# Performance work log

Hardware: AMD Instinct MI355X
Metric: run time of the kernel (lower is better)

Reference implementation:

```python
import jax, jax.numpy as jnp
import numpy as np

N = 50000      # nodes
E = 800000     # edges (before self-loops)
DIN = 64
DH = 64
DOUT = 64
G = 500        # graphs in batch
EPS = 1e-5     # BatchNorm eps


def setup_inputs() -> dict:
    key = jax.random.key(0)
    ks = jax.random.split(key, 8)
    x = jax.random.normal(ks[0], (N, DIN), dtype=jnp.float32)
    edge_index = jax.random.randint(ks[1], (2, E), 0, N, dtype=jnp.int32)
    batch = jnp.sort(jax.random.randint(ks[2], (N,), 0, G, dtype=jnp.int32))

    def lin(k, di, do):
        return (jax.random.normal(k, (di, do), dtype=jnp.float32) / np.float32(np.sqrt(di)))

    inp = dict(x=x, edge_index=edge_index, batch=batch)
    dims = [(DIN, DH), (DH, DH), (DH, DOUT)]
    for i, (di, do) in enumerate(dims, start=1):
        inp[f"W{i}"] = lin(ks[2 + i], di, do)
        inp[f"b{i}"] = jnp.zeros((do,), jnp.float32)
        inp[f"gamma{i}"] = jnp.ones((do,), jnp.float32)
        inp[f"beta{i}"] = jnp.zeros((do,), jnp.float32)
    return inp


def _gcn_norm(edge_index, n_nodes):
    # add self loops, compute symmetric normalization deg^-1/2 * deg^-1/2
    loop = jnp.arange(n_nodes, dtype=edge_index.dtype)
    src = jnp.concatenate([edge_index[0], loop])
    dst = jnp.concatenate([edge_index[1], loop])
    deg = jax.ops.segment_sum(jnp.ones_like(dst, dtype=jnp.float32), dst,
                              num_segments=n_nodes)
    dinv = jax.lax.rsqrt(deg)  # deg >= 1 thanks to self-loops
    norm = dinv[src] * dinv[dst]  # [E + N]
    return src, dst, norm


def _gcn_conv(x, src, dst, norm, W, b, n_nodes):
    h = x @ W                               # [N, dout]
    msg = h[src] * norm[:, None]            # gather + scale  [E+N, dout]
    out = jax.ops.segment_sum(msg, dst, num_segments=n_nodes)  # scatter-add
    return out + b


def _batchnorm(x, gamma, beta):
    mean = jnp.mean(x, axis=0)
    var = jnp.mean(jnp.square(x - mean), axis=0)  # biased, as in torch training BN
    return gamma * (x - mean) * jax.lax.rsqrt(var + EPS) + beta


def reference(x, edge_index, batch, W1, b1, gamma1, beta1,
              W2, b2, gamma2, beta2, W3, b3, gamma3, beta3):
    src, dst, norm = _gcn_norm(edge_index, N)
    layers = [(W1, b1, gamma1, beta1), (W2, b2, gamma2, beta2),
              (W3, b3, gamma3, beta3)]
    h = x
    for i, (W, b, g, be) in enumerate(layers):
        h = _gcn_conv(h, src, dst, norm, W, b, N)
        h = _batchnorm(h, g, be)
        if i < len(layers) - 1:
            h = jax.nn.relu(h)  # dropout is identity in eval / reference
    # global mean pool over graphs
    sums = jax.ops.segment_sum(h, batch, num_segments=G)          # [G, DOUT]
    cnts = jax.ops.segment_sum(jnp.ones((N,), jnp.float32), batch,
                               num_segments=G)
    return sums / jnp.maximum(cnts, 1.0)[:, None]
```

## Files before the change

kernel.cpp:

```cpp
#include <hip/hip_runtime.h>
#include <hip/hip_fp16.h>

#define BN_EPS 1e-5f
#define CCH 4096
#define NSLICE 32
#define OUT_CAP 8192
#define CAP 8192
#define SXS 68


__device__ inline __half2 u2h(unsigned u) {
    union { unsigned u; __half2 h; } x; x.u = u; return x.h;
}
__device__ inline unsigned h2u(__half2 h) {
    union { unsigned u; __half2 h; } x; x.h = h; return x.u;
}
__device__ inline unsigned pack_f16x2(float a, float b) {
    return h2u(__floats2half2_rn(a, b));
}


__global__ __launch_bounds__(256) void scatter_direct(const int* __restrict__ src,
                                                      const int* __restrict__ dst,
                                                      int* __restrict__ ccnt,
                                                      unsigned* __restrict__ tmp,
                                                      float* __restrict__ cnt_g,
                                                      float* __restrict__ out,
                                                      int E, int G) {
    __shared__ int lcnt[256];
    int t = threadIdx.x;
    int tid = blockIdx.x * 256 + t;
    int stride = gridDim.x * 256;
    for (int i = tid; i < G * 64; i += stride) out[i] = 0.f;
    for (int i = tid; i < G; i += stride) cnt_g[i] = 0.f;

    int e0 = blockIdx.x * CCH;
    lcnt[t] = 0;
    __syncthreads();
#pragma unroll
    for (int k = 0; k < CCH / 256; ++k) {
        int e = e0 + k * 256 + t;
        if (e < E) atomicAdd(&lcnt[dst[e] >> 8], 1);
    }
    __syncthreads();
    int c = lcnt[t];
    __syncthreads();
    if (c > 0) lcnt[t] = t * CAP + atomicAdd(&ccnt[t], c);
    __syncthreads();
#pragma unroll
    for (int k = 0; k < CCH / 256; ++k) {
        int e = e0 + k * 256 + t;
        if (e < E) {
            int d = dst[e];
            int pos = atomicAdd(&lcnt[d >> 8], 1);
            tmp[pos] = ((unsigned)src[e] << 8) | (unsigned)(d & 255);
        }
    }
}


__global__ __launch_bounds__(256) void build_csr(const unsigned* __restrict__ tmp,
                                                 const int* __restrict__ ccnt,
                                                 int* __restrict__ rp,
                                                 unsigned short* __restrict__ deg,
                                                 unsigned short* __restrict__ col,
                                                 float* __restrict__ dinv,
                                                 const int* __restrict__ batch,
                                                 float* __restrict__ cnt_g,
                                                 int n, int G) {
    __shared__ int hist[256];
    __shared__ int sc[256];
    __shared__ unsigned short outw[OUT_CAP];
    __shared__ int h[512];
    int b = blockIdx.x;
    int t = threadIdx.x;
    int beg = b * CAP;
    int m = ccnt[b];
    int end = beg + m;
    hist[t] = 0;
    __syncthreads();
    for (int e = beg + t; e < end; e += 256) atomicAdd(&hist[tmp[e] & 255u], 1);
    __syncthreads();
    int v = hist[t];
    sc[t] = v;
    __syncthreads();
    for (int off = 1; off < 256; off <<= 1) {
        int u = (t >= off) ? sc[t - off] : 0;
        __syncthreads();
        sc[t] += u;
        __syncthreads();
    }
    int excl = sc[t] - v;
    int node = b * 256 + t;
    if (node < n) {
        dinv[node] = rsqrtf(1.0f + (float)v);
        rp[node] = beg + excl;
        deg[node] = (unsigned short)v;
    }
    hist[t] = excl;
    __syncthreads();
    if (m <= OUT_CAP) {
        for (int e = beg + t; e < end; e += 256) {
            unsigned p = tmp[e];
            int pos = atomicAdd(&hist[p & 255u], 1);
            outw[pos] = (unsigned short)(p >> 8);
        }
        __syncthreads();
        for (int i = t; i < m; i += 256) col[beg + i] = outw[i];
    } else {
        for (int e = beg + t; e < end; e += 256) {
            unsigned p = tmp[e];
            int pos = atomicAdd(&hist[p & 255u], 1);
            col[beg + pos] = (unsigned short)(p >> 8);
        }
    }
    if (G <= 512) {
        __syncthreads();
        for (int i = t; i < 512; i += 256) h[i] = 0;
        __syncthreads();
        for (int i = b * 256 + t; i < n; i += gridDim.x * 256)
            atomicAdd(&h[batch[i]], 1);
        __syncthreads();
        for (int i = t; i < G; i += 256)
            if (h[i]) atomicAdd(&cnt_g[i], (float)h[i]);
    } else {
        for (int i = b * 256 + t; i < n; i += gridDim.x * 256)
            atomicAdd(&cnt_g[batch[i]], 1.0f);
    }
}


__global__ __launch_bounds__(256) void gemm64_v2(const float* __restrict__ X,
                                                 const float* __restrict__ W,
                                                 const float* __restrict__ dinv,
                                                 const float* __restrict__ part,
                                                 const float* __restrict__ gamma,
                                                 const float* __restrict__ beta,
                                                 int has_bn, float inv_n,
                                                 unsigned* __restrict__ Hs, int n) {
    __shared__ float sX[64 * SXS];
    __shared__ float sW[64 * SXS];
    __shared__ float s_scsh[128];
    int t = threadIdx.x;
    int c4 = t & 15;
    int base = blockIdx.x * 64;

    if (has_bn) {
        if (t < 128) {
            float s = 0.f;
#pragma unroll
            for (int k = 0; k < NSLICE; ++k) s += part[k * 128 + t];
            s_scsh[t] = s;
        }
        __syncthreads();
        if (t < 64) {
            float mean = s_scsh[t] * inv_n;
            float var = s_scsh[64 + t] * inv_n - mean * mean;
            float sc = gamma[t] * rsqrtf(var + BN_EPS);
            s_scsh[t] = sc;
            s_scsh[64 + t] = beta[t] - mean * sc;
        }
        __syncthreads();
    }

    {
        const float4* W4 = (const float4*)W;
#pragma unroll
        for (int it = 0; it < 4; ++it) {
            int idx = it * 256 + t;
            int r = idx >> 4;
            float4 v = W4[r * 16 + c4];
            *(float4*)&sW[r * SXS + c4 * 4] = v;
        }
    }
    {
        const float4* X4 = (const float4*)X;
        float4 sc4, sh4;
        if (has_bn) {
            sc4 = *(const float4*)&s_scsh[c4 * 4];
            sh4 = *(const float4*)&s_scsh[64 + c4 * 4];
        }
#pragma unroll
        for (int it = 0; it < 4; ++it) {
            int idx = it * 256 + t;
            int r = idx >> 4;
            int grow = base + r;
            float4 v = make_float4(0.f, 0.f, 0.f, 0.f);
            if (grow < n) v = X4[(size_t)grow * 16 + c4];
            if (has_bn) {
                v.x = fmaxf(fmaf(v.x, sc4.x, sh4.x), 0.f);
                v.y = fmaxf(fmaf(v.y, sc4.y, sh4.y), 0.f);
                v.z = fmaxf(fmaf(v.z, sc4.z, sh4.z), 0.f);
                v.w = fmaxf(fmaf(v.w, sc4.w, sh4.w), 0.f);
            }
            *(float4*)&sX[r * SXS + c4 * 4] = v;
        }
    }
    __syncthreads();

    int rgrp = t >> 4;
    float4 acc[4];
#pragma unroll
    for (int ri = 0; ri < 4; ++ri) acc[ri] = make_float4(0.f, 0.f, 0.f, 0.f);

#pragma unroll 4
    for (int k4 = 0; k4 < 16; ++k4) {
        float4 xv[4], wv[4];
#pragma unroll
        for (int ri = 0; ri < 4; ++ri)
            xv[ri] = *(const float4*)&sX[(rgrp + 16 * ri) * SXS + k4 * 4];
#pragma unroll
        for (int kk = 0; kk < 4; ++kk)
            wv[kk] = *(const float4*)&sW[(k4 * 4 + kk) * SXS + c4 * 4];
#pragma unroll
        for (int ri = 0; ri < 4; ++ri) {
            acc[ri].x = fmaf(xv[ri].x, wv[0].x, acc[ri].x);
            acc[ri].y = fmaf(xv[ri].x, wv[0].y, acc[ri].y);
            acc[ri].z = fmaf(xv[ri].x, wv[0].z, acc[ri].z);
            acc[ri].w = fmaf(xv[ri].x, wv[0].w, acc[ri].w);
            acc[ri].x = fmaf(xv[ri].y, wv[1].x, acc[ri].x);
            acc[ri].y = fmaf(xv[ri].y, wv[1].y, acc[ri].y);
            acc[ri].z = fmaf(xv[ri].y, wv[1].z, acc[ri].z);
            acc[ri].w = fmaf(xv[ri].y, wv[1].w, acc[ri].w);
            acc[ri].x = fmaf(xv[ri].z, wv[2].x, acc[ri].x);
            acc[ri].y = fmaf(xv[ri].z, wv[2].y, acc[ri].y);
            acc[ri].z = fmaf(xv[ri].z, wv[2].z, acc[ri].z);
            acc[ri].w = fmaf(xv[ri].z, wv[2].w, acc[ri].w);
            acc[ri].x = fmaf(xv[ri].w, wv[3].x, acc[ri].x);
            acc[ri].y = fmaf(xv[ri].w, wv[3].y, acc[ri].y);
            acc[ri].z = fmaf(xv[ri].w, wv[3].z, acc[ri].z);
            acc[ri].w = fmaf(xv[ri].w, wv[3].w, acc[ri].w);
        }
    }

#pragma unroll
    for (int ri = 0; ri < 4; ++ri) {
        int row = base + rgrp + 16 * ri;
        if (row < n) {
            float dv = dinv[row];
            uint2 o2;
            o2.x = pack_f16x2(acc[ri].x * dv, acc[ri].y * dv);
            o2.y = pack_f16x2(acc[ri].z * dv, acc[ri].w * dv);
            ((uint2*)Hs)[(size_t)row * 16 + c4] = o2;
        }
    }
}


__global__ __launch_bounds__(256) void agg(const uint4* __restrict__ Hs4,
                                           const int* __restrict__ rp,
                                           const unsigned short* __restrict__ deg,
                                           const unsigned short* __restrict__ col,
                                           const float* __restrict__ dinv,
                                           float* __restrict__ Y,
                                           float* __restrict__ part, int n) {
    __shared__ float sS[4][64];
    __shared__ float sQ[4][64];
    int t = threadIdx.x;
    int w = t >> 6;
    int lane = t & 63;
    int g = lane >> 3;
    int c = lane & 7;
    int d = blockIdx.x * 4 + w;
    bool valid = d < n;
    int dc = valid ? d : 0;
    __half2 a0 = u2h(0u), a1 = u2h(0u), a2 = u2h(0u), a3 = u2h(0u);
    int beg = 0, end = 0;
    if (valid) { beg = rp[dc]; end = beg + (int)deg[dc]; }
    for (int b = beg; b < end; b += 64) {
        int m = min(64, end - b);
        int myidx = (lane < m) ? (int)col[b + lane] : 0;
        int jj = 0;
        for (; jj + 15 < m; jj += 16) {
            int s0 = __shfl(myidx, jj + g, 64);
            int s1 = __shfl(myidx, jj + 8 + g, 64);
            uint4 v0 = Hs4[(size_t)s0 * 8 + c];
            uint4 v1 = Hs4[(size_t)s1 * 8 + c];
            a0 = __hadd2(a0, u2h(v0.x)); a1 = __hadd2(a1, u2h(v0.y));
            a2 = __hadd2(a2, u2h(v0.z)); a3 = __hadd2(a3, u2h(v0.w));
            a0 = __hadd2(a0, u2h(v1.x)); a1 = __hadd2(a1, u2h(v1.y));
            a2 = __hadd2(a2, u2h(v1.z)); a3 = __hadd2(a3, u2h(v1.w));
        }
        for (; jj < m; jj += 8) {
            int e = jj + g;
            int s0 = __shfl(myidx, e, 64);
            if (e < m) {
                uint4 v = Hs4[(size_t)s0 * 8 + c];
                a0 = __hadd2(a0, u2h(v.x)); a1 = __hadd2(a1, u2h(v.y));
                a2 = __hadd2(a2, u2h(v.z)); a3 = __hadd2(a3, u2h(v.w));
            }
        }
    }
#pragma unroll
    for (int mask = 8; mask <= 32; mask <<= 1) {
        a0 = __hadd2(a0, u2h((unsigned)__shfl_xor((int)h2u(a0), mask, 64)));
        a1 = __hadd2(a1, u2h((unsigned)__shfl_xor((int)h2u(a1), mask, 64)));
        a2 = __hadd2(a2, u2h((unsigned)__shfl_xor((int)h2u(a2), mask, 64)));
        a3 = __hadd2(a3, u2h((unsigned)__shfl_xor((int)h2u(a3), mask, 64)));
    }
    if (g == 0) {
        float2 f0 = __half22float2(a0), f1 = __half22float2(a1);
        float2 f2 = __half22float2(a2), f3 = __half22float2(a3);
        float y0 = f0.x, y1 = f0.y, y2 = f1.x, y3 = f1.y;
        float y4 = f2.x, y5 = f2.y, y6 = f3.x, y7 = f3.y;
        if (valid) {
            uint4 hv = Hs4[(size_t)dc * 8 + c];
            float2 h0 = __half22float2(u2h(hv.x)), h1 = __half22float2(u2h(hv.y));
            float2 h2v = __half22float2(u2h(hv.z)), h3 = __half22float2(u2h(hv.w));
            float dv = dinv[dc];
            y0 = (y0 + h0.x) * dv; y1 = (y1 + h0.y) * dv;
            y2 = (y2 + h1.x) * dv; y3 = (y3 + h1.y) * dv;
            y4 = (y4 + h2v.x) * dv; y5 = (y5 + h2v.y) * dv;
            y6 = (y6 + h3.x) * dv; y7 = (y7 + h3.y) * dv;
            *(float4*)&Y[(size_t)dc * 64 + c * 8]     = make_float4(y0, y1, y2, y3);
            *(float4*)&Y[(size_t)dc * 64 + c * 8 + 4] = make_float4(y4, y5, y6, y7);
        } else {
            y0 = y1 = y2 = y3 = y4 = y5 = y6 = y7 = 0.f;
        }
        *(float4*)&sS[w][c * 8]     = make_float4(y0, y1, y2, y3);
        *(float4*)&sS[w][c * 8 + 4] = make_float4(y4, y5, y6, y7);
        *(float4*)&sQ[w][c * 8]     = make_float4(y0 * y0, y1 * y1, y2 * y2, y3 * y3);
        *(float4*)&sQ[w][c * 8 + 4] = make_float4(y4 * y4, y5 * y5, y6 * y6, y7 * y7);
    }
    __syncthreads();
    if (t < 64) {
        float s = sS[0][t] + sS[1][t] + sS[2][t] + sS[3][t];
        float qq = sQ[0][t] + sQ[1][t] + sQ[2][t] + sQ[3][t];
        float* dst = part + (size_t)(blockIdx.x & (NSLICE - 1)) * 128;
        atomicAdd(&dst[t], s);
        atomicAdd(&dst[64 + t], qq);
    }
}

__global__ __launch_bounds__(256) void agg_pool(const uint4* __restrict__ Hs4,
                                                const int* __restrict__ rp,
                                                const unsigned short* __restrict__ deg,
                                                const unsigned short* __restrict__ col,
                                                const float* __restrict__ dinv,
                                                const int* __restrict__ batch,
                                                float* __restrict__ out,
                                                float* __restrict__ part, int n) {
    __shared__ float sS[4][64];
    __shared__ float sQ[4][64];
    __shared__ int sG[4];
    int t = threadIdx.x;
    int w = t >> 6;
    int lane = t & 63;
    int g = lane >> 3;
    int c = lane & 7;
    int d = blockIdx.x * 4 + w;
    bool valid = d < n;
    int dc = valid ? d : 0;
    __half2 a0 = u2h(0u), a1 = u2h(0u), a2 = u2h(0u), a3 = u2h(0u);
    int beg = 0, end = 0;
    if (valid) { beg = rp[dc]; end = beg + (int)deg[dc]; }
    for (int b = beg; b < end; b += 64) {
        int m = min(64, end - b);
        int myidx = (lane < m) ? (int)col[b + lane] : 0;
        int jj = 0;
        for (; jj + 15 < m; jj += 16) {
            int s0 = __shfl(myidx, jj + g, 64);
            int s1 = __shfl(myidx, jj + 8 + g, 64);
            uint4 v0 = Hs4[(size_t)s0 * 8 + c];
            uint4 v1 = Hs4[(size_t)s1 * 8 + c];
            a0 = __hadd2(a0, u2h(v0.x)); a1 = __hadd2(a1, u2h(v0.y));
            a2 = __hadd2(a2, u2h(v0.z)); a3 = __hadd2(a3, u2h(v0.w));
            a0 = __hadd2(a0, u2h(v1.x)); a1 = __hadd2(a1, u2h(v1.y));
            a2 = __hadd2(a2, u2h(v1.z)); a3 = __hadd2(a3, u2h(v1.w));
        }
        for (; jj < m; jj += 8) {
            int e = jj + g;
            int s0 = __shfl(myidx, e, 64);
            if (e < m) {
                uint4 v = Hs4[(size_t)s0 * 8 + c];
                a0 = __hadd2(a0, u2h(v.x)); a1 = __hadd2(a1, u2h(v.y));
                a2 = __hadd2(a2, u2h(v.z)); a3 = __hadd2(a3, u2h(v.w));
            }
        }
    }
#pragma unroll
    for (int mask = 8; mask <= 32; mask <<= 1) {
        a0 = __hadd2(a0, u2h((unsigned)__shfl_xor((int)h2u(a0), mask, 64)));
        a1 = __hadd2(a1, u2h((unsigned)__shfl_xor((int)h2u(a1), mask, 64)));
        a2 = __hadd2(a2, u2h((unsigned)__shfl_xor((int)h2u(a2), mask, 64)));
        a3 = __hadd2(a3, u2h((unsigned)__shfl_xor((int)h2u(a3), mask, 64)));
    }
    if (g == 0) {
        float2 f0 = __half22float2(a0), f1 = __half22float2(a1);
        float2 f2 = __half22float2(a2), f3 = __half22float2(a3);
        float y0 = f0.x, y1 = f0.y, y2 = f1.x, y3 = f1.y;
        float y4 = f2.x, y5 = f2.y, y6 = f3.x, y7 = f3.y;
        if (valid) {
            uint4 hv = Hs4[(size_t)dc * 8 + c];
            float2 h0 = __half22float2(u2h(hv.x)), h1 = __half22float2(u2h(hv.y));
            float2 h2v = __half22float2(u2h(hv.z)), h3 = __half22float2(u2h(hv.w));
            float dv = dinv[dc];
            y0 = (y0 + h0.x) * dv; y1 = (y1 + h0.y) * dv;
            y2 = (y2 + h1.x) * dv; y3 = (y3 + h1.y) * dv;
            y4 = (y4 + h2v.x) * dv; y5 = (y5 + h2v.y) * dv;
            y6 = (y6 + h3.x) * dv; y7 = (y7 + h3.y) * dv;
        } else {
            y0 = y1 = y2 = y3 = y4 = y5 = y6 = y7 = 0.f;
        }
        *(float4*)&sS[w][c * 8]     = make_float4(y0, y1, y2, y3);
        *(float4*)&sS[w][c * 8 + 4] = make_float4(y4, y5, y6, y7);
        *(float4*)&sQ[w][c * 8]     = make_float4(y0 * y0, y1 * y1, y2 * y2, y3 * y3);
        *(float4*)&sQ[w][c * 8 + 4] = make_float4(y4 * y4, y5 * y5, y6 * y6, y7 * y7);
        if (lane == 0) sG[w] = valid ? batch[dc] : -1;
    }
    __syncthreads();
    if (t < 64) {
        float s = sS[0][t] + sS[1][t] + sS[2][t] + sS[3][t];
        float qq = sQ[0][t] + sQ[1][t] + sQ[2][t] + sQ[3][t];
        float* dst = part + (size_t)(blockIdx.x & (NSLICE - 1)) * 128;
        atomicAdd(&dst[t], s);
        atomicAdd(&dst[64 + t], qq);
        int g0 = sG[0], g1 = sG[1], g2 = sG[2], g3 = sG[3];
        if (g0 >= 0 && g0 == g1 && g0 == g2 && g0 == g3) {
            atomicAdd(&out[(size_t)g0 * 64 + t], s);
        } else {
            if (g0 >= 0) atomicAdd(&out[(size_t)g0 * 64 + t], sS[0][t]);
            if (g1 >= 0) atomicAdd(&out[(size_t)g1 * 64 + t], sS[1][t]);
            if (g2 >= 0) atomicAdd(&out[(size_t)g2 * 64 + t], sS[2][t]);
            if (g3 >= 0) atomicAdd(&out[(size_t)g3 * 64 + t], sS[3][t]);
        }
    }
}


__global__ __launch_bounds__(256) void pool_div(float* __restrict__ out,
                                                const float* __restrict__ cnt,
                                                const float* __restrict__ part,
                                                const float* __restrict__ gamma,
                                                const float* __restrict__ beta,
                                                int G, float inv_n) {
    __shared__ float s_scsh[128];
    int t = threadIdx.x;
    if (t < 128) {
        float s = 0.f;
#pragma unroll
        for (int k = 0; k < NSLICE; ++k) s += part[k * 128 + t];
        s_scsh[t] = s;
    }
    __syncthreads();
    if (t < 64) {
        float mean = s_scsh[t] * inv_n;
        float var = s_scsh[64 + t] * inv_n - mean * mean;
        float sc = gamma[t] * rsqrtf(var + BN_EPS);
        s_scsh[t] = sc;
        s_scsh[64 + t] = beta[t] - mean * sc;
    }
    __syncthreads();
    int idx = blockIdx.x * 256 + t;
    if (idx >= G * 64) return;
    int j = idx & 63, g = idx >> 6;
    float c = cnt[g];
    out[idx] = (c > 0.5f) ? fmaf(s_scsh[j], out[idx] / c, s_scsh[64 + j]) : 0.f;
}


extern "C" void kernel_launch(void* const* d_in, const int* in_sizes, int n_in,
                              void* d_out, int out_size, void* d_ws, size_t ws_size,
                              hipStream_t stream) {
    const float* x     = (const float*)d_in[0];
    const int*   ei    = (const int*)d_in[1];
    const int*   batch = (const int*)d_in[2];
    const float* Wl[3] = {(const float*)d_in[3], (const float*)d_in[7], (const float*)d_in[11]};
    const float* gl[3] = {(const float*)d_in[5], (const float*)d_in[9], (const float*)d_in[13]};
    const float* bl[3] = {(const float*)d_in[6], (const float*)d_in[10], (const float*)d_in[14]};
    float* out = (float*)d_out;

    int E = in_sizes[1] / 2;
    int n = in_sizes[0] / 64;
    int G = out_size / 64;
    const int* src = ei;
    const int* dst = ei + E;
    int NBC = (n + 255) / 256;
    float inv_n = 1.0f / (float)n;

    char* ws = (char*)d_ws;
    size_t off = 0;
    auto carve = [&](size_t bytes) {
        void* p = ws + off;
        off += (bytes + 255) & ~(size_t)255;
        return p;
    };
    float*          part  = (float*)carve(3 * NSLICE * 128 * 4);
    int*            ccnt  = (int*)carve(256 * 4);
    float*          dinv  = (float*)carve((size_t)n * 4);
    float*          cnt_g = (float*)carve((size_t)G * 4);
    unsigned*       Hs    = (unsigned*)carve((size_t)n * 32 * 4);
    float*          Ybuf  = (float*)carve((size_t)n * 64 * 4);
    int*            rp    = (int*)carve(((size_t)n + 1) * 4);
    unsigned short* deg   = (unsigned short*)carve((size_t)n * 2);
    unsigned*       tmp   = (unsigned*)carve((size_t)NBC * CAP * 4);
    unsigned short* col   = (unsigned short*)carve((size_t)NBC * CAP * 2);

    int pgrid = (E + CCH - 1) / CCH;
    int gemm_grid = (n + 63) / 64;
    int agg_grid = (n + 3) / 4;

    hipMemsetAsync(part, 0, 3 * NSLICE * 128 * 4 + 256 * 4, stream);
    scatter_direct<<<pgrid, 256, 0, stream>>>(src, dst, ccnt, tmp, cnt_g, out, E, G);
    build_csr<<<NBC, 256, 0, stream>>>(tmp, ccnt, rp, deg, col, dinv, batch, cnt_g, n, G);

    const float* cur = x;
    for (int l = 0; l < 3; ++l) {
        float* part_l = part + (size_t)l * NSLICE * 128;
        const float* part_prev = (l > 0) ? part + (size_t)(l - 1) * NSLICE * 128 : part;
        gemm64_v2<<<gemm_grid, 256, 0, stream>>>(cur, Wl[l], dinv, part_prev,
                                                 l > 0 ? gl[l - 1] : gl[0],
                                                 l > 0 ? bl[l - 1] : bl[0],
                                                 l > 0 ? 1 : 0, inv_n, Hs, n);
        if (l < 2) {
            agg<<<agg_grid, 256, 0, stream>>>((const uint4*)Hs, rp, deg, col, dinv,
                                              Ybuf, part_l, n);
        } else {
            agg_pool<<<agg_grid, 256, 0, stream>>>((const uint4*)Hs, rp, deg, col, dinv,
                                                   batch, out, part_l, n);
        }
        cur = Ybuf;
    }

    pool_div<<<(G * 64 + 255) / 256, 256, 0, stream>>>(out, cnt_g,
                                                       part + 2 * NSLICE * 128,
                                                       gl[2], bl[2], G, inv_n);
}
```

Measured before the change: 241.0 us.

## Assign two nodes per wavefront in aggregation and batch eight gathers per chunk

The aggregation kernels now give each half-wavefront (32 lanes) its own destination node, so a block of 256 threads covers eight nodes instead of four. Each 32-edge chunk issues all eight row gathers into registers before accumulating. The aim is to cut idle lanes for low-degree nodes (average degree about 17) and to raise memory-level parallelism. The costs are more registers per thread, more shared-memory slots, and a longer per-block reduction and pooling loop over eight slots.

```diff
diff --git a/kernel.cpp b/kernel.cpp
--- a/kernel.cpp
+++ b/kernel.cpp
@@ -254,51 +254,48 @@
                                            const float* __restrict__ dinv,
                                            float* __restrict__ Y,
                                            float* __restrict__ part, int n) {
-    __shared__ float sS[4][64];
-    __shared__ float sQ[4][64];
+    __shared__ float sS[8][64];
+    __shared__ float sQ[8][64];
     int t = threadIdx.x;
     int w = t >> 6;
     int lane = t & 63;
-    int g = lane >> 3;
-    int c = lane & 7;
-    int d = blockIdx.x * 4 + w;
+    int h = lane >> 5;
+    int l5 = lane & 31;
+    int g4 = l5 >> 3;
+    int c = l5 & 7;
+    int d = blockIdx.x * 8 + w * 2 + h;
     bool valid = d < n;
     int dc = valid ? d : 0;
     __half2 a0 = u2h(0u), a1 = u2h(0u), a2 = u2h(0u), a3 = u2h(0u);
     int beg = 0, end = 0;
     if (valid) { beg = rp[dc]; end = beg + (int)deg[dc]; }
-    for (int b = beg; b < end; b += 64) {
-        int m = min(64, end - b);
-        int myidx = (lane < m) ? (int)col[b + lane] : 0;
-        int jj = 0;
-        for (; jj + 15 < m; jj += 16) {
-            int s0 = __shfl(myidx, jj + g, 64);
-            int s1 = __shfl(myidx, jj + 8 + g, 64);
-            uint4 v0 = Hs4[(size_t)s0 * 8 + c];
-            uint4 v1 = Hs4[(size_t)s1 * 8 + c];
-            a0 = __hadd2(a0, u2h(v0.x)); a1 = __hadd2(a1, u2h(v0.y));
-            a2 = __hadd2(a2, u2h(v0.z)); a3 = __hadd2(a3, u2h(v0.w));
-            a0 = __hadd2(a0, u2h(v1.x)); a1 = __hadd2(a1, u2h(v1.y));
-            a2 = __hadd2(a2, u2h(v1.z)); a3 = __hadd2(a3, u2h(v1.w));
-        }
-        for (; jj < m; jj += 8) {
-            int e = jj + g;
-            int s0 = __shfl(myidx, e, 64);
+    for (int b = beg; b < end; b += 32) {
+        int m = min(32, end - b);
+        int myidx = (l5 < m) ? (int)col[b + l5] : 0;
+        uint4 v[8];
+#pragma unroll
+        for (int k = 0; k < 8; ++k) {
+            int e = 4 * k + g4;
+            int s0 = __shfl(myidx, e, 32);
+            if (e < m) v[k] = Hs4[(size_t)s0 * 8 + c];
+        }
+#pragma unroll
+        for (int k = 0; k < 8; ++k) {
+            int e = 4 * k + g4;
             if (e < m) {
-                uint4 v = Hs4[(size_t)s0 * 8 + c];
-                a0 = __hadd2(a0, u2h(v.x)); a1 = __hadd2(a1, u2h(v.y));
-                a2 = __hadd2(a2, u2h(v.z)); a3 = __hadd2(a3, u2h(v.w));
+                a0 = __hadd2(a0, u2h(v[k].x)); a1 = __hadd2(a1, u2h(v[k].y));
+                a2 = __hadd2(a2, u2h(v[k].z)); a3 = __hadd2(a3, u2h(v[k].w));
             }
         }
     }
 #pragma unroll
-    for (int mask = 8; mask <= 32; mask <<= 1) {
+    for (int mask = 8; mask <= 16; mask <<= 1) {
         a0 = __hadd2(a0, u2h((unsigned)__shfl_xor((int)h2u(a0), mask, 64)));
         a1 = __hadd2(a1, u2h((unsigned)__shfl_xor((int)h2u(a1), mask, 64)));
         a2 = __hadd2(a2, u2h((unsigned)__shfl_xor((int)h2u(a2), mask, 64)));
         a3 = __hadd2(a3, u2h((unsigned)__shfl_xor((int)h2u(a3), mask, 64)));
     }
-    if (g == 0) {
+    if (g4 == 0) {
         float2 f0 = __half22float2(a0), f1 = __half22float2(a1);
         float2 f2 = __half22float2(a2), f3 = __half22float2(a3);
         float y0 = f0.x, y1 = f0.y, y2 = f1.x, y3 = f1.y;
@@ -317,15 +314,17 @@
         } else {
             y0 = y1 = y2 = y3 = y4 = y5 = y6 = y7 = 0.f;
         }
-        *(float4*)&sS[w][c * 8]     = make_float4(y0, y1, y2, y3);
-        *(float4*)&sS[w][c * 8 + 4] = make_float4(y4, y5, y6, y7);
-        *(float4*)&sQ[w][c * 8]     = make_float4(y0 * y0, y1 * y1, y2 * y2, y3 * y3);
-        *(float4*)&sQ[w][c * 8 + 4] = make_float4(y4 * y4, y5 * y5, y6 * y6, y7 * y7);
+        int slot = w * 2 + h;
+        *(float4*)&sS[slot][c * 8]     = make_float4(y0, y1, y2, y3);
+        *(float4*)&sS[slot][c * 8 + 4] = make_float4(y4, y5, y6, y7);
+        *(float4*)&sQ[slot][c * 8]     = make_float4(y0 * y0, y1 * y1, y2 * y2, y3 * y3);
+        *(float4*)&sQ[slot][c * 8 + 4] = make_float4(y4 * y4, y5 * y5, y6 * y6, y7 * y7);
     }
     __syncthreads();
     if (t < 64) {
-        float s = sS[0][t] + sS[1][t] + sS[2][t] + sS[3][t];
-        float qq = sQ[0][t] + sQ[1][t] + sQ[2][t] + sQ[3][t];
+        float s = 0.f, qq = 0.f;
+#pragma unroll
+        for (int i = 0; i < 8; ++i) { s += sS[i][t]; qq += sQ[i][t]; }
         float* dst = part + (size_t)(blockIdx.x & (NSLICE - 1)) * 128;
         atomicAdd(&dst[t], s);
         atomicAdd(&dst[64 + t], qq);
@@ -340,52 +339,49 @@
                                                 const int* __restrict__ batch,
                                                 float* __restrict__ out,
                                                 float* __restrict__ part, int n) {
-    __shared__ float sS[4][64];
-    __shared__ float sQ[4][64];
-    __shared__ int sG[4];
+    __shared__ float sS[8][64];
+    __shared__ float sQ[8][64];
+    __shared__ int sG[8];
     int t = threadIdx.x;
     int w = t >> 6;
     int lane = t & 63;
-    int g = lane >> 3;
-    int c = lane & 7;
-    int d = blockIdx.x * 4 + w;
+    int h = lane >> 5;
+    int l5 = lane & 31;
+    int g4 = l5 >> 3;
+    int c = l5 & 7;
+    int d = blockIdx.x * 8 + w * 2 + h;
     bool valid = d < n;
     int dc = valid ? d : 0;
     __half2 a0 = u2h(0u), a1 = u2h(0u), a2 = u2h(0u), a3 = u2h(0u);
     int beg = 0, end = 0;
     if (valid) { beg = rp[dc]; end = beg + (int)deg[dc]; }
-    for (int b = beg; b < end; b += 64) {
-        int m = min(64, end - b);
-        int myidx = (lane < m) ? (int)col[b + lane] : 0;
-        int jj = 0;
-        for (; jj + 15 < m; jj += 16) {
-            int s0 = __shfl(myidx, jj + g, 64);
-            int s1 = __shfl(myidx, jj + 8 + g, 64);
-            uint4 v0 = Hs4[(size_t)s0 * 8 + c];
-            uint4 v1 = Hs4[(size_t)s1 * 8 + c];
-            a0 = __hadd2(a0, u2h(v0.x)); a1 = __hadd2(a1, u2h(v0.y));
-            a2 = __hadd2(a2, u2h(v0.z)); a3 = __hadd2(a3, u2h(v0.w));
-            a0 = __hadd2(a0, u2h(v1.x)); a1 = __hadd2(a1, u2h(v1.y));
-            a2 = __hadd2(a2, u2h(v1.z)); a3 = __hadd2(a3, u2h(v1.w));
-        }
-        for (; jj < m; jj += 8) {
-            int e = jj + g;
-            int s0 = __shfl(myidx, e, 64);
+    for (int b = beg; b < end; b += 32) {
+        int m = min(32, end - b);
+        int myidx = (l5 < m) ? (int)col[b + l5] : 0;
+        uint4 v[8];
+#pragma unroll
+        for (int k = 0; k < 8; ++k) {
+            int e = 4 * k + g4;
+            int s0 = __shfl(myidx, e, 32);
+            if (e < m) v[k] = Hs4[(size_t)s0 * 8 + c];
+        }
+#pragma unroll
+        for (int k = 0; k < 8; ++k) {
+            int e = 4 * k + g4;
             if (e < m) {
-                uint4 v = Hs4[(size_t)s0 * 8 + c];
-                a0 = __hadd2(a0, u2h(v.x)); a1 = __hadd2(a1, u2h(v.y));
-                a2 = __hadd2(a2, u2h(v.z)); a3 = __hadd2(a3, u2h(v.w));
+                a0 = __hadd2(a0, u2h(v[k].x)); a1 = __hadd2(a1, u2h(v[k].y));
+                a2 = __hadd2(a2, u2h(v[k].z)); a3 = __hadd2(a3, u2h(v[k].w));
             }
         }
     }
 #pragma unroll
-    for (int mask = 8; mask <= 32; mask <<= 1) {
+    for (int mask = 8; mask <= 16; mask <<= 1) {
         a0 = __hadd2(a0, u2h((unsigned)__shfl_xor((int)h2u(a0), mask, 64)));
         a1 = __hadd2(a1, u2h((unsigned)__shfl_xor((int)h2u(a1), mask, 64)));
         a2 = __hadd2(a2, u2h((unsigned)__shfl_xor((int)h2u(a2), mask, 64)));
         a3 = __hadd2(a3, u2h((unsigned)__shfl_xor((int)h2u(a3), mask, 64)));
     }
-    if (g == 0) {
+    if (g4 == 0) {
         float2 f0 = __half22float2(a0), f1 = __half22float2(a1);
         float2 f2 = __half22float2(a2), f3 = __half22float2(a3);
         float y0 = f0.x, y1 = f0.y, y2 = f1.x, y3 = f1.y;
@@ -402,27 +398,33 @@
         } else {
             y0 = y1 = y2 = y3 = y4 = y5 = y6 = y7 = 0.f;
         }
-        *(float4*)&sS[w][c * 8]     = make_float4(y0, y1, y2, y3);
-        *(float4*)&sS[w][c * 8 + 4] = make_float4(y4, y5, y6, y7);
-        *(float4*)&sQ[w][c * 8]     = make_float4(y0 * y0, y1 * y1, y2 * y2, y3 * y3);
-        *(float4*)&sQ[w][c * 8 + 4] = make_float4(y4 * y4, y5 * y5, y6 * y6, y7 * y7);
-        if (lane == 0) sG[w] = valid ? batch[dc] : -1;
+        int slot = w * 2 + h;
+        *(float4*)&sS[slot][c * 8]     = make_float4(y0, y1, y2, y3);
+        *(float4*)&sS[slot][c * 8 + 4] = make_float4(y4, y5, y6, y7);
+        *(float4*)&sQ[slot][c * 8]     = make_float4(y0 * y0, y1 * y1, y2 * y2, y3 * y3);
+        *(float4*)&sQ[slot][c * 8 + 4] = make_float4(y4 * y4, y5 * y5, y6 * y6, y7 * y7);
+        if (l5 == 0) sG[slot] = valid ? batch[dc] : -1;
     }
     __syncthreads();
     if (t < 64) {
-        float s = sS[0][t] + sS[1][t] + sS[2][t] + sS[3][t];
-        float qq = sQ[0][t] + sQ[1][t] + sQ[2][t] + sQ[3][t];
+        float s = 0.f, qq = 0.f;
+#pragma unroll
+        for (int i = 0; i < 8; ++i) { s += sS[i][t]; qq += sQ[i][t]; }
         float* dst = part + (size_t)(blockIdx.x & (NSLICE - 1)) * 128;
         atomicAdd(&dst[t], s);
         atomicAdd(&dst[64 + t], qq);
-        int g0 = sG[0], g1 = sG[1], g2 = sG[2], g3 = sG[3];
-        if (g0 >= 0 && g0 == g1 && g0 == g2 && g0 == g3) {
+        int g0 = sG[0];
+        bool same = (g0 >= 0);
+#pragma unroll
+        for (int i = 1; i < 8; ++i) same = same && (sG[i] == g0);
+        if (same) {
             atomicAdd(&out[(size_t)g0 * 64 + t], s);
         } else {
-            if (g0 >= 0) atomicAdd(&out[(size_t)g0 * 64 + t], sS[0][t]);
-            if (g1 >= 0) atomicAdd(&out[(size_t)g1 * 64 + t], sS[1][t]);
-            if (g2 >= 0) atomicAdd(&out[(size_t)g2 * 64 + t], sS[2][t]);
-            if (g3 >= 0) atomicAdd(&out[(size_t)g3 * 64 + t], sS[3][t]);
+#pragma unroll
+            for (int i = 0; i < 8; ++i) {
+                int gi = sG[i];
+                if (gi >= 0) atomicAdd(&out[(size_t)gi * 64 + t], sS[i][t]);
+            }
         }
     }
 }
@@ -498,7 +500,7 @@
 
     int pgrid = (E + CCH - 1) / CCH;
     int gemm_grid = (n + 63) / 64;
-    int agg_grid = (n + 3) / 4;
+    int agg_grid = (n + 7) / 8;
 
     hipMemsetAsync(part, 0, 3 * NSLICE * 128 * 4 + 256 * 4, stream);
     scatter_direct<<<pgrid, 256, 0, stream>>>(src, dst, ccnt, tmp, cnt_g, out, E, G);
```

Result: faster. 229.1 us (-4.9%).
